# Optimization experiments

Measured on AMD Instinct MI355X. Metric: run time of the kernel, lower is better.

Reference implementation:

```python
import jax, jax.numpy as jnp
import numpy as np

B, S, D, H = 2, 2048, 1024, 16
DH = D // H
NEG = -1000000000.0


def setup_inputs() -> dict:
    key = jax.random.key(0)
    ks = jax.random.split(key, 8)
    q = jax.random.normal(ks[0], (B, S, D), dtype=jnp.float32)
    k = jax.random.normal(ks[1], (B, S, D), dtype=jnp.float32)
    v = jax.random.normal(ks[2], (B, S, D), dtype=jnp.float32)
    # padding mask [B, k_len]; ensure first key position is valid
    mask = jax.random.randint(ks[3], (B, S), 0, 2, dtype=jnp.int32)
    mask = mask.at[:, 0].set(1)
    scale = 1.0 / np.sqrt(D)
    Wq = jax.random.normal(ks[4], (D, D), dtype=jnp.float32) * scale
    Wk = jax.random.normal(ks[5], (D, D), dtype=jnp.float32) * scale
    Wv = jax.random.normal(ks[6], (D, D), dtype=jnp.float32) * scale
    Wo = jax.random.normal(ks[7], (D, D), dtype=jnp.float32) * scale
    return {"q": q, "k": k, "v": v, "mask": mask,
            "Wq": Wq, "Wk": Wk, "Wv": Wv, "Wo": Wo}


def reference(q, k, v, mask, Wq, Wk, Wv, Wo):
    # nn.Linear(bias=False): y = x @ W.T  (W is [out, in])
    Q = jnp.einsum('bsd,ed->bse', q, Wq)
    K = jnp.einsum('bsd,ed->bse', k, Wk)
    V = jnp.einsum('bsd,ed->bse', v, Wv)
    # split heads -> [B, H, S, DH]
    Q = Q.reshape(B, S, H, DH).transpose(0, 2, 1, 3)
    K = K.reshape(B, S, H, DH).transpose(0, 2, 1, 3)
    V = V.reshape(B, S, H, DH).transpose(0, 2, 1, 3)
    scores = jnp.einsum('bhqd,bhkd->bhqk', Q, K) / jnp.float32(np.sqrt(DH))
    # padding mask: [B, K] -> additive [B, 1, 1, K]
    pad = jnp.where(mask == 0, jnp.float32(NEG), jnp.float32(0.0))[:, None, None, :]
    scores = scores + pad
    # causal (mask_future=True): strict upper triangle blocked
    causal = jnp.where(jnp.triu(jnp.ones((S, S), dtype=bool), k=1),
                       jnp.float32(NEG), jnp.float32(0.0))
    scores = scores + causal
    attn = jax.nn.softmax(scores, axis=-1)
    out = jnp.einsum('bhqk,bhkd->bhqd', attn, V)  # [B, H, S, DH]
    out = out.transpose(0, 2, 1, 3).reshape(B, S, D)
    out = jnp.einsum('bsd,ed->bse', out, Wo)
    # dropout: identity in eval mode
    return out
```

## Files before the change

kernel.cpp:

```cpp
#include <hip/hip_runtime.h>
#include <stdint.h>

#define BB 2
#define SS 2048
#define DD 1024
#define HH 16
#define DHH 64

typedef __bf16 bf16_t;
typedef bf16_t bf16x8 __attribute__((ext_vector_type(8)));
typedef float f32x4 __attribute__((ext_vector_type(4)));
typedef short s16x4 __attribute__((ext_vector_type(4)));

union FragU { uint4 u; bf16x8 b; };
union Frag4U { uint2 u; s16x4 s; };

#if __has_builtin(__builtin_amdgcn_exp2f)
#define EXP2(x) __builtin_amdgcn_exp2f(x)
#else
#define EXP2(x) exp2f(x)
#endif

__device__ __forceinline__ unsigned short f2bf(float f) {
  union { float f; unsigned int u; } x; x.f = f;
  unsigned int u = x.u;
  return (unsigned short)((u + 0x7FFFu + ((u >> 16) & 1u)) >> 16);
}

__device__ __forceinline__ uint2 pack4(float4 v) {
  uint2 r;
  r.x = (unsigned)f2bf(v.x) | ((unsigned)f2bf(v.y) << 16);
  r.y = (unsigned)f2bf(v.z) | ((unsigned)f2bf(v.w) << 16);
  return r;
}

__device__ __forceinline__ bf16x8 ldsFrag(const unsigned short* s, int idx) {
  FragU f;
  f.u = *reinterpret_cast<const uint4*>(s + idx);
  return f.b;
}

__device__ __forceinline__ void gload_lds16(const unsigned short* g, unsigned short* s) {
  __builtin_amdgcn_global_load_lds(
      (const __attribute__((address_space(1))) unsigned int*)g,
      (__attribute__((address_space(3))) unsigned int*)s, 16, 0, 0);
}

#define MFMA16(a, b, c) __builtin_amdgcn_mfma_f32_16x16x32_bf16((a), (b), (c), 0, 0, 0)
#define MFMA16K16(a, b, c) __builtin_amdgcn_mfma_f32_16x16x16bf16_1k((a), (b), (c), 0, 0, 0)

__global__ __launch_bounds__(256) void convert_kernel(
    const float* __restrict__ q, const float* __restrict__ k, const float* __restrict__ v,
    const float* __restrict__ Wq, const float* __restrict__ Wk,
    const float* __restrict__ Wv, const float* __restrict__ Wo,
    const int* __restrict__ mask,
    unsigned short* __restrict__ Ab, unsigned short* __restrict__ Wb,
    float* __restrict__ Mf) {
  const int z = blockIdx.y;
  if (z == 7) {
    if (blockIdx.x >= 4) return;
    const size_t base = (size_t)blockIdx.x * 1024 + (size_t)threadIdx.x * 4;
    int4 m4 = *reinterpret_cast<const int4*>(mask + base);
    float4 p;
    p.x = (m4.x == 0) ? -1.0e9f : 0.0f;
    p.y = (m4.y == 0) ? -1.0e9f : 0.0f;
    p.z = (m4.z == 0) ? -1.0e9f : 0.0f;
    p.w = (m4.w == 0) ? -1.0e9f : 0.0f;
    *reinterpret_cast<float4*>(Mf + base) = p;
    return;
  }
  const float* src;
  unsigned short* dst;
  float scale = 1.0f;
  if (z < 3) {
    src = (z == 0) ? q : (z == 1) ? k : v;
    dst = Ab + (size_t)z * BB * SS * DD;
  } else {
    if (blockIdx.x >= (DD * DD / 1024)) return;
    src = (z == 3) ? Wq : (z == 4) ? Wk : (z == 5) ? Wv : Wo;
    dst = Wb + (size_t)(z - 3) * DD * DD;
    if (z == 3) scale = 0.125f * 1.44269504088896f;
  }
  const size_t base = (size_t)blockIdx.x * 1024 + (size_t)threadIdx.x * 4;
  float4 val = *reinterpret_cast<const float4*>(src + base);
  val.x *= scale; val.y *= scale; val.z *= scale; val.w *= scale;
  uint2 p = pack4(val);
  *reinterpret_cast<uint2*>(dst + base) = p;
}

__global__ __launch_bounds__(256) void proj128_kernel(
    const unsigned short* __restrict__ Ab, const unsigned short* __restrict__ Wb,
    unsigned short* __restrict__ Qb, unsigned short* __restrict__ Kb,
    unsigned short* __restrict__ Vt) {
  __shared__ unsigned short sA[128 * 64];
  __shared__ unsigned short sB[128 * 64];

  const int z = blockIdx.z;
  const unsigned short* A = Ab + (size_t)z * BB * SS * DD;
  const unsigned short* W = Wb + (size_t)z * DD * DD;
  unsigned short* Out = (z == 0) ? Qb : (z == 1) ? Kb : Vt;
  const int layout = (z == 2) ? 1 : 0;

  const int t = threadIdx.x;
  const int lane = t & 63, wave = t >> 6;
  const int quad = lane >> 4, l15 = lane & 15;
  const int wr = wave >> 1, wc = wave & 1;
  const int mBase = blockIdx.x * 128, nBase = blockIdx.y * 128;

  f32x4 acc[4][4] = {};

  for (int k0 = 0; k0 < DD; k0 += 64) {
    #pragma unroll
    for (int i = 0; i < 4; ++i) {
      const int g = wave * 4 + i;
      const int row = g * 8 + (lane >> 3);
      const int oct = (lane & 7) ^ (row & 7);
      gload_lds16(A + (size_t)(mBase + row) * DD + k0 + oct * 8, &sA[g * 512]);
      gload_lds16(W + (size_t)(nBase + row) * DD + k0 + oct * 8, &sB[g * 512]);
    }
    __syncthreads();

    #pragma unroll
    for (int kk = 0; kk < 2; ++kk) {
      bf16x8 af[4], bfr[4];
      #pragma unroll
      for (int i = 0; i < 4; ++i) {
        const int row = wr * 64 + i * 16 + l15;
        af[i] = ldsFrag(sA, (row * 8 + ((kk * 4 + quad) ^ (l15 & 7))) * 8);
      }
      #pragma unroll
      for (int j = 0; j < 4; ++j) {
        const int row = wc * 64 + j * 16 + l15;
        bfr[j] = ldsFrag(sB, (row * 8 + ((kk * 4 + quad) ^ (l15 & 7))) * 8);
      }
      #pragma unroll
      for (int i = 0; i < 4; ++i)
        #pragma unroll
        for (int j = 0; j < 4; ++j)
          acc[i][j] = MFMA16(af[i], bfr[j], acc[i][j]);
    }
    __syncthreads();
  }

  #pragma unroll
  for (int i = 0; i < 4; ++i) {
    #pragma unroll
    for (int j = 0; j < 4; ++j) {
      #pragma unroll
      for (int r = 0; r < 4; ++r) {
        int m = mBase + wr * 64 + i * 16 + quad * 4 + r;
        int n = nBase + wc * 64 + j * 16 + l15;
        int b = m >> 11, s = m & (SS - 1);
        int h = n >> 6, dh = n & (DHH - 1);
        size_t off;
        if (layout == 0)
          off = ((size_t)(b * HH + h) * SS + s) * DHH + dh;
        else
          off = ((size_t)(b * HH + h) * DHH + dh) * SS + s;
        Out[off] = f2bf(acc[i][j][r]);
      }
    }
  }
}

__global__ __launch_bounds__(256, 4) void attn_kernel(
    const unsigned short* __restrict__ Qb, const unsigned short* __restrict__ Kb,
    const unsigned short* __restrict__ Vt, const float* __restrict__ Mf,
    unsigned short* __restrict__ Ob) {
  __shared__ __align__(16) char smem[32768];
  unsigned short* sK = (unsigned short*)smem;
  unsigned short* sV = (unsigned short*)(smem + 16384);
  unsigned short* sO = (unsigned short*)smem;

  const int t = threadIdx.x;
  const int lane = t & 63, wave = t >> 6;
  const int quad = lane >> 4, l15 = lane & 15;

  const int id = blockIdx.x;
  const int xcd = id & 7, rest = id >> 3;
  const int hd = xcd * 4 + (rest >> 5);
  const int qt = 31 - (rest & 31);
  const int b = hd >> 4, h = hd & 15;
  const int qb = qt * 64;

  const size_t headOff = (size_t)hd * SS * DHH;
  const unsigned short* Qh = Qb + headOff;
  const unsigned short* Kh = Kb + headOff;
  const unsigned short* Vh = Vt + headOff;
  const float* Mp = Mf + b * SS;

  bf16x8 aq[2];
  {
    const unsigned short* qp = Qh + (size_t)(qb + wave * 16 + l15) * DHH + quad * 8;
    FragU f0, f1;
    f0.u = *reinterpret_cast<const uint4*>(qp);
    f1.u = *reinterpret_cast<const uint4*>(qp + 32);
    aq[0] = f0.b; aq[1] = f1.b;
  }

  float m_l = -1.0e30f, l_l = 0.0f;
  f32x4 oacc[4] = {};
  const int nc = (qt + 2) >> 1;
  const int qrow_abs = qb + wave * 16 + l15;

  for (int c = 0; c < nc; ++c) {
    const int c0 = c * 128;
    #pragma unroll
    for (int i = 0; i < 4; ++i) {
      const int g = wave * 4 + i;
      const int row = g * 8 + (lane >> 3);
      const int oct = (lane & 7) ^ (row & 7);
      gload_lds16(Kh + (size_t)(c0 + row) * DHH + oct * 8, &sK[g * 512]);
    }
    #pragma unroll
    for (int i = 0; i < 4; ++i) {
      const int g = wave * 4 + i;
      const int row = g * 4 + (lane >> 4);
      const int oct = (lane & 15) ^ (row & 15);
      gload_lds16(Vh + (size_t)row * SS + c0 + oct * 8, &sV[g * 512]);
    }
    __syncthreads();

    f32x4 sacc[8] = {};
    #pragma unroll
    for (int kk = 0; kk < 2; ++kk) {
      #pragma unroll
      for (int j = 0; j < 8; ++j) {
        const int row = j * 16 + l15;
        bf16x8 ak = ldsFrag(sK, (row * 8 + ((kk * 4 + quad) ^ (l15 & 7))) * 8);
        sacc[j] = MFMA16(ak, aq[kk], sacc[j]);
      }
    }

    float rm = -1.0e30f;
    #pragma unroll
    for (int j = 0; j < 8; ++j)
      rm = fmaxf(rm, fmaxf(fmaxf(sacc[j][0], sacc[j][1]), fmaxf(sacc[j][2], sacc[j][3])));
    rm = fmaxf(rm, __shfl_xor(rm, 16));
    rm = fmaxf(rm, __shfl_xor(rm, 32));
    const float mnew = fmaxf(m_l, rm);
    const float alpha = EXP2(m_l - mnew);
    m_l = mnew;

    const bool diag = (c == nc - 1);
    float rs = 0.0f;
    s16x4 pk[8];
    #pragma unroll
    for (int j = 0; j < 8; ++j) {
      float4 pf = *reinterpret_cast<const float4*>(Mp + c0 + j * 16 + quad * 4);
      float p0 = EXP2(sacc[j][0] - mnew + pf.x);
      float p1 = EXP2(sacc[j][1] - mnew + pf.y);
      float p2 = EXP2(sacc[j][2] - mnew + pf.z);
      float p3 = EXP2(sacc[j][3] - mnew + pf.w);
      if (diag) {
        const int key = c0 + j * 16 + quad * 4;
        p0 = (key + 0 > qrow_abs) ? 0.0f : p0;
        p1 = (key + 1 > qrow_abs) ? 0.0f : p1;
        p2 = (key + 2 > qrow_abs) ? 0.0f : p2;
        p3 = (key + 3 > qrow_abs) ? 0.0f : p3;
      }
      rs += (p0 + p1) + (p2 + p3);
      Frag4U fu;
      fu.u.x = __builtin_amdgcn_perm(__float_as_uint(p1) + 0x8000u,
                                     __float_as_uint(p0) + 0x8000u, 0x07060302u);
      fu.u.y = __builtin_amdgcn_perm(__float_as_uint(p3) + 0x8000u,
                                     __float_as_uint(p2) + 0x8000u, 0x07060302u);
      pk[j] = fu.s;
    }
    rs += __shfl_xor(rs, 16);
    rs += __shfl_xor(rs, 32);
    l_l = l_l * alpha + rs;

    #pragma unroll
    for (int jn = 0; jn < 4; ++jn)
      oacc[jn] *= alpha;

    #pragma unroll
    for (int j = 0; j < 8; ++j) {
      #pragma unroll
      for (int jn = 0; jn < 4; ++jn) {
        const int row = jn * 16 + l15;
        const int unit = row * 16 + ((2 * j + (quad >> 1)) ^ l15);
        Frag4U av;
        av.u = *reinterpret_cast<const uint2*>(&sV[unit * 8 + (quad & 1) * 4]);
        oacc[jn] = MFMA16K16(av.s, pk[j], oacc[jn]);
      }
    }
    __syncthreads();
  }

  const float inv = 1.0f / l_l;
  #pragma unroll
  for (int jn = 0; jn < 4; ++jn) {
    uint2 w;
    w.x = (unsigned)f2bf(oacc[jn][0] * inv) | ((unsigned)f2bf(oacc[jn][1] * inv) << 16);
    w.y = (unsigned)f2bf(oacc[jn][2] * inv) | ((unsigned)f2bf(oacc[jn][3] * inv) << 16);
    *reinterpret_cast<uint2*>(&sO[(wave * 16 + l15) * 72 + jn * 16 + quad * 4]) = w;
  }
  __syncthreads();
  {
    const int row = t >> 2, seg = t & 3;
    uint4 u0 = *reinterpret_cast<const uint4*>(&sO[row * 72 + seg * 16]);
    uint4 u1 = *reinterpret_cast<const uint4*>(&sO[row * 72 + seg * 16 + 8]);
    unsigned short* dst = Ob + (size_t)(b * SS + qb + row) * DD + h * DHH + seg * 16;
    *reinterpret_cast<uint4*>(dst) = u0;
    *reinterpret_cast<uint4*>(dst + 8) = u1;
  }
}

__global__ __launch_bounds__(256) void outproj_kernel(
    const unsigned short* __restrict__ Ag, const unsigned short* __restrict__ Wb,
    float* __restrict__ Out) {
  __shared__ unsigned short sA[128 * 64];
  __shared__ unsigned short sB[128 * 64];

  const unsigned short* W = Wb + (size_t)3 * DD * DD;
  const int t = threadIdx.x;
  const int lane = t & 63, wave = t >> 6;
  const int quad = lane >> 4, l15 = lane & 15;
  const int wr = wave >> 1, wc = wave & 1;
  const int mBase = blockIdx.x * 128, nBase = blockIdx.y * 128;

  f32x4 acc[4][4] = {};

  for (int k0 = 0; k0 < DD; k0 += 64) {
    #pragma unroll
    for (int i = 0; i < 4; ++i) {
      const int g = wave * 4 + i;
      const int row = g * 8 + (lane >> 3);
      const int oct = (lane & 7) ^ (row & 7);
      gload_lds16(Ag + (size_t)(mBase + row) * DD + k0 + oct * 8, &sA[g * 512]);
      gload_lds16(W + (size_t)(nBase + row) * DD + k0 + oct * 8, &sB[g * 512]);
    }
    __syncthreads();

    #pragma unroll
    for (int kk = 0; kk < 2; ++kk) {
      bf16x8 af[4], bfr[4];
      #pragma unroll
      for (int i = 0; i < 4; ++i) {
        const int row = wr * 64 + i * 16 + l15;
        af[i] = ldsFrag(sA, (row * 8 + ((kk * 4 + quad) ^ (l15 & 7))) * 8);
      }
      #pragma unroll
      for (int j = 0; j < 4; ++j) {
        const int row = wc * 64 + j * 16 + l15;
        bfr[j] = ldsFrag(sB, (row * 8 + ((kk * 4 + quad) ^ (l15 & 7))) * 8);
      }
      #pragma unroll
      for (int i = 0; i < 4; ++i)
        #pragma unroll
        for (int j = 0; j < 4; ++j)
          acc[i][j] = MFMA16(af[i], bfr[j], acc[i][j]);
    }
    __syncthreads();
  }

  #pragma unroll
  for (int i = 0; i < 4; ++i) {
    #pragma unroll
    for (int j = 0; j < 4; ++j) {
      #pragma unroll
      for (int r = 0; r < 4; ++r) {
        int m = mBase + wr * 64 + i * 16 + quad * 4 + r;
        int n = nBase + wc * 64 + j * 16 + l15;
        Out[(size_t)m * DD + n] = acc[i][j][r];
      }
    }
  }
}

extern "C" void kernel_launch(void* const* d_in, const int* in_sizes, int n_in,
                              void* d_out, int out_size, void* d_ws, size_t ws_size,
                              hipStream_t stream) {
  (void)in_sizes; (void)n_in; (void)out_size; (void)ws_size;
  const float* q  = (const float*)d_in[0];
  const float* k  = (const float*)d_in[1];
  const float* v  = (const float*)d_in[2];
  const int* mask = (const int*)d_in[3];
  const float* Wq = (const float*)d_in[4];
  const float* Wk = (const float*)d_in[5];
  const float* Wv = (const float*)d_in[6];
  const float* Wo = (const float*)d_in[7];
  float* out = (float*)d_out;

  const size_t AE = (size_t)BB * SS * DD;
  unsigned short* Ab = (unsigned short*)d_ws;
  unsigned short* Ob = Ab;
  unsigned short* Wb = Ab + 3 * AE;
  unsigned short* Qb = Wb + (size_t)4 * DD * DD;
  unsigned short* Kb = Qb + AE;
  unsigned short* Vt = Kb + AE;
  float* Mf = (float*)(Vt + AE);

  convert_kernel<<<dim3(AE / 1024, 8), 256, 0, stream>>>(
      q, k, v, Wq, Wk, Wv, Wo, mask, Ab, Wb, Mf);

  proj128_kernel<<<dim3(BB * SS / 128, DD / 128, 3), 256, 0, stream>>>(
      Ab, Wb, Qb, Kb, Vt);

  attn_kernel<<<dim3(32 * HH * BB), 256, 0, stream>>>(Qb, Kb, Vt, Mf, Ob);

  outproj_kernel<<<dim3(BB * SS / 128, DD / 128), 256, 0, stream>>>(Ob, Wb, out);
}
```

Baseline: 254.3 us.

## Double-buffer LDS in projection, attention and out-proj with smaller tiles

```diff
diff --git a/kernel.cpp b/kernel.cpp
--- a/kernel.cpp
+++ b/kernel.cpp
@@ -88,12 +88,12 @@
   *reinterpret_cast<uint2*>(dst + base) = p;
 }
 
-__global__ __launch_bounds__(256) void proj128_kernel(
+__global__ __launch_bounds__(256, 3) void proj_kernel(
     const unsigned short* __restrict__ Ab, const unsigned short* __restrict__ Wb,
     unsigned short* __restrict__ Qb, unsigned short* __restrict__ Kb,
     unsigned short* __restrict__ Vt) {
-  __shared__ unsigned short sA[128 * 64];
-  __shared__ unsigned short sB[128 * 64];
+  __shared__ unsigned short sA[2][64 * 64];
+  __shared__ unsigned short sB[2][128 * 64];
 
   const int z = blockIdx.z;
   const unsigned short* A = Ab + (size_t)z * BB * SS * DD;
@@ -105,50 +105,75 @@
   const int lane = t & 63, wave = t >> 6;
   const int quad = lane >> 4, l15 = lane & 15;
   const int wr = wave >> 1, wc = wave & 1;
-  const int mBase = blockIdx.x * 128, nBase = blockIdx.y * 128;
-
-  f32x4 acc[4][4] = {};
-
-  for (int k0 = 0; k0 < DD; k0 += 64) {
-    #pragma unroll
-    for (int i = 0; i < 4; ++i) {
-      const int g = wave * 4 + i;
-      const int row = g * 8 + (lane >> 3);
-      const int oct = (lane & 7) ^ (row & 7);
-      gload_lds16(A + (size_t)(mBase + row) * DD + k0 + oct * 8, &sA[g * 512]);
-      gload_lds16(W + (size_t)(nBase + row) * DD + k0 + oct * 8, &sB[g * 512]);
-    }
+  const int mBase = blockIdx.x * 64, nBase = blockIdx.y * 128;
+  const int srow = lane >> 3, soct = lane & 7;
+
+  f32x4 acc[2][4] = {};
+
+  #pragma unroll
+  for (int i = 0; i < 2; ++i) {
+    const int g = wave * 2 + i;
+    const int row = g * 8 + srow;
+    const int oct = soct ^ (row & 7);
+    gload_lds16(A + (size_t)(mBase + row) * DD + oct * 8, &sA[0][g * 512]);
+  }
+  #pragma unroll
+  for (int i = 0; i < 4; ++i) {
+    const int g = wave * 4 + i;
+    const int row = g * 8 + srow;
+    const int oct = soct ^ (row & 7);
+    gload_lds16(W + (size_t)(nBase + row) * DD + oct * 8, &sB[0][g * 512]);
+  }
+
+  for (int kt = 0; kt < DD / 64; ++kt) {
     __syncthreads();
-
+    if (kt + 1 < DD / 64) {
+      const int k1 = (kt + 1) * 64;
+      const int nb = (kt + 1) & 1;
+      #pragma unroll
+      for (int i = 0; i < 2; ++i) {
+        const int g = wave * 2 + i;
+        const int row = g * 8 + srow;
+        const int oct = soct ^ (row & 7);
+        gload_lds16(A + (size_t)(mBase + row) * DD + k1 + oct * 8, &sA[nb][g * 512]);
+      }
+      #pragma unroll
+      for (int i = 0; i < 4; ++i) {
+        const int g = wave * 4 + i;
+        const int row = g * 8 + srow;
+        const int oct = soct ^ (row & 7);
+        gload_lds16(W + (size_t)(nBase + row) * DD + k1 + oct * 8, &sB[nb][g * 512]);
+      }
+    }
+    const int cb = kt & 1;
     #pragma unroll
     for (int kk = 0; kk < 2; ++kk) {
-      bf16x8 af[4], bfr[4];
-      #pragma unroll
-      for (int i = 0; i < 4; ++i) {
-        const int row = wr * 64 + i * 16 + l15;
-        af[i] = ldsFrag(sA, (row * 8 + ((kk * 4 + quad) ^ (l15 & 7))) * 8);
+      bf16x8 af[2], bfr[4];
+      #pragma unroll
+      for (int i = 0; i < 2; ++i) {
+        const int row = wr * 32 + i * 16 + l15;
+        af[i] = ldsFrag(sA[cb], (row * 8 + ((kk * 4 + quad) ^ (l15 & 7))) * 8);
       }
       #pragma unroll
       for (int j = 0; j < 4; ++j) {
         const int row = wc * 64 + j * 16 + l15;
-        bfr[j] = ldsFrag(sB, (row * 8 + ((kk * 4 + quad) ^ (l15 & 7))) * 8);
-      }
-      #pragma unroll
-      for (int i = 0; i < 4; ++i)
+        bfr[j] = ldsFrag(sB[cb], (row * 8 + ((kk * 4 + quad) ^ (l15 & 7))) * 8);
+      }
+      #pragma unroll
+      for (int i = 0; i < 2; ++i)
         #pragma unroll
         for (int j = 0; j < 4; ++j)
           acc[i][j] = MFMA16(af[i], bfr[j], acc[i][j]);
     }
-    __syncthreads();
-  }
-
-  #pragma unroll
-  for (int i = 0; i < 4; ++i) {
+  }
+
+  #pragma unroll
+  for (int i = 0; i < 2; ++i) {
     #pragma unroll
     for (int j = 0; j < 4; ++j) {
       #pragma unroll
       for (int r = 0; r < 4; ++r) {
-        int m = mBase + wr * 64 + i * 16 + quad * 4 + r;
+        int m = mBase + wr * 32 + i * 16 + quad * 4 + r;
         int n = nBase + wc * 64 + j * 16 + l15;
         int b = m >> 11, s = m & (SS - 1);
         int h = n >> 6, dh = n & (DHH - 1);
@@ -166,11 +191,10 @@
 __global__ __launch_bounds__(256, 4) void attn_kernel(
     const unsigned short* __restrict__ Qb, const unsigned short* __restrict__ Kb,
     const unsigned short* __restrict__ Vt, const float* __restrict__ Mf,
-    unsigned short* __restrict__ Ob) {
-  __shared__ __align__(16) char smem[32768];
-  unsigned short* sK = (unsigned short*)smem;
-  unsigned short* sV = (unsigned short*)(smem + 16384);
-  unsigned short* sO = (unsigned short*)smem;
+    unsigned short* __restrict__ Obh) {
+  __shared__ __align__(16) unsigned short sK[2][64 * 64];
+  __shared__ __align__(16) unsigned short sV[2][64 * 64];
+  unsigned short* sO = &sK[0][0];
 
   const int t = threadIdx.x;
   const int lane = t & 63, wave = t >> 6;
@@ -180,7 +204,7 @@
   const int xcd = id & 7, rest = id >> 3;
   const int hd = xcd * 4 + (rest >> 5);
   const int qt = 31 - (rest & 31);
-  const int b = hd >> 4, h = hd & 15;
+  const int b = hd >> 4;
   const int qb = qt * 64;
 
   const size_t headOff = (size_t)hd * SS * DHH;
@@ -198,43 +222,52 @@
     aq[0] = f0.b; aq[1] = f1.b;
   }
 
+  const int srow = lane >> 3, soct = lane & 7;
+
+  #pragma unroll
+  for (int i = 0; i < 2; ++i) {
+    const int g = wave * 2 + i;
+    const int row = g * 8 + srow;
+    const int oct = soct ^ (row & 7);
+    gload_lds16(Kh + (size_t)row * DHH + oct * 8, &sK[0][g * 512]);
+    gload_lds16(Vh + (size_t)row * SS + oct * 8, &sV[0][g * 512]);
+  }
+
   float m_l = -1.0e30f, l_l = 0.0f;
   f32x4 oacc[4] = {};
-  const int nc = (qt + 2) >> 1;
   const int qrow_abs = qb + wave * 16 + l15;
 
-  for (int c = 0; c < nc; ++c) {
-    const int c0 = c * 128;
-    #pragma unroll
-    for (int i = 0; i < 4; ++i) {
-      const int g = wave * 4 + i;
-      const int row = g * 8 + (lane >> 3);
-      const int oct = (lane & 7) ^ (row & 7);
-      gload_lds16(Kh + (size_t)(c0 + row) * DHH + oct * 8, &sK[g * 512]);
-    }
-    #pragma unroll
-    for (int i = 0; i < 4; ++i) {
-      const int g = wave * 4 + i;
-      const int row = g * 4 + (lane >> 4);
-      const int oct = (lane & 15) ^ (row & 15);
-      gload_lds16(Vh + (size_t)row * SS + c0 + oct * 8, &sV[g * 512]);
-    }
+  for (int c = 0; c <= qt; ++c) {
     __syncthreads();
-
-    f32x4 sacc[8] = {};
+    if (c < qt) {
+      const int c1 = (c + 1) * 64;
+      const int nb = (c + 1) & 1;
+      #pragma unroll
+      for (int i = 0; i < 2; ++i) {
+        const int g = wave * 2 + i;
+        const int row = g * 8 + srow;
+        const int oct = soct ^ (row & 7);
+        gload_lds16(Kh + (size_t)(c1 + row) * DHH + oct * 8, &sK[nb][g * 512]);
+        gload_lds16(Vh + (size_t)row * SS + c1 + oct * 8, &sV[nb][g * 512]);
+      }
+    }
+    const int cb = c & 1;
+    const int c0 = c * 64;
+
+    f32x4 sacc[4] = {};
     #pragma unroll
     for (int kk = 0; kk < 2; ++kk) {
       #pragma unroll
-      for (int j = 0; j < 8; ++j) {
+      for (int j = 0; j < 4; ++j) {
         const int row = j * 16 + l15;
-        bf16x8 ak = ldsFrag(sK, (row * 8 + ((kk * 4 + quad) ^ (l15 & 7))) * 8);
+        bf16x8 ak = ldsFrag(sK[cb], (row * 8 + ((kk * 4 + quad) ^ (l15 & 7))) * 8);
         sacc[j] = MFMA16(ak, aq[kk], sacc[j]);
       }
     }
 
     float rm = -1.0e30f;
     #pragma unroll
-    for (int j = 0; j < 8; ++j)
+    for (int j = 0; j < 4; ++j)
       rm = fmaxf(rm, fmaxf(fmaxf(sacc[j][0], sacc[j][1]), fmaxf(sacc[j][2], sacc[j][3])));
     rm = fmaxf(rm, __shfl_xor(rm, 16));
     rm = fmaxf(rm, __shfl_xor(rm, 32));
@@ -242,11 +275,11 @@
     const float alpha = EXP2(m_l - mnew);
     m_l = mnew;
 
-    const bool diag = (c == nc - 1);
+    const bool diag = (c == qt);
     float rs = 0.0f;
-    s16x4 pk[8];
-    #pragma unroll
-    for (int j = 0; j < 8; ++j) {
+    s16x4 pk[4];
+    #pragma unroll
+    for (int j = 0; j < 4; ++j) {
       float4 pf = *reinterpret_cast<const float4*>(Mp + c0 + j * 16 + quad * 4);
       float p0 = EXP2(sacc[j][0] - mnew + pf.x);
       float p1 = EXP2(sacc[j][1] - mnew + pf.y);
@@ -276,19 +309,19 @@
       oacc[jn] *= alpha;
 
     #pragma unroll
-    for (int j = 0; j < 8; ++j) {
+    for (int j = 0; j < 4; ++j) {
       #pragma unroll
       for (int jn = 0; jn < 4; ++jn) {
         const int row = jn * 16 + l15;
-        const int unit = row * 16 + ((2 * j + (quad >> 1)) ^ l15);
+        const int oct = (2 * j + (quad >> 1)) ^ (l15 & 7);
         Frag4U av;
-        av.u = *reinterpret_cast<const uint2*>(&sV[unit * 8 + (quad & 1) * 4]);
+        av.u = *reinterpret_cast<const uint2*>(&sV[cb][(row * 8 + oct) * 8 + (quad & 1) * 4]);
         oacc[jn] = MFMA16K16(av.s, pk[j], oacc[jn]);
       }
     }
-    __syncthreads();
-  }
-
+  }
+
+  __syncthreads();
   const float inv = 1.0f / l_l;
   #pragma unroll
   for (int jn = 0; jn < 4; ++jn) {
@@ -302,67 +335,97 @@
     const int row = t >> 2, seg = t & 3;
     uint4 u0 = *reinterpret_cast<const uint4*>(&sO[row * 72 + seg * 16]);
     uint4 u1 = *reinterpret_cast<const uint4*>(&sO[row * 72 + seg * 16 + 8]);
-    unsigned short* dst = Ob + (size_t)(b * SS + qb + row) * DD + h * DHH + seg * 16;
+    unsigned short* dst = Obh + headOff + (size_t)(qb + row) * DHH + seg * 16;
     *reinterpret_cast<uint4*>(dst) = u0;
     *reinterpret_cast<uint4*>(dst + 8) = u1;
   }
 }
 
-__global__ __launch_bounds__(256) void outproj_kernel(
-    const unsigned short* __restrict__ Ag, const unsigned short* __restrict__ Wb,
+__global__ __launch_bounds__(256, 3) void outproj_kernel(
+    const unsigned short* __restrict__ Obh, const unsigned short* __restrict__ Wb,
     float* __restrict__ Out) {
-  __shared__ unsigned short sA[128 * 64];
-  __shared__ unsigned short sB[128 * 64];
+  __shared__ unsigned short sA[2][64 * 64];
+  __shared__ unsigned short sB[2][128 * 64];
 
   const unsigned short* W = Wb + (size_t)3 * DD * DD;
   const int t = threadIdx.x;
   const int lane = t & 63, wave = t >> 6;
   const int quad = lane >> 4, l15 = lane & 15;
   const int wr = wave >> 1, wc = wave & 1;
-  const int mBase = blockIdx.x * 128, nBase = blockIdx.y * 128;
-
-  f32x4 acc[4][4] = {};
-
-  for (int k0 = 0; k0 < DD; k0 += 64) {
-    #pragma unroll
-    for (int i = 0; i < 4; ++i) {
-      const int g = wave * 4 + i;
-      const int row = g * 8 + (lane >> 3);
-      const int oct = (lane & 7) ^ (row & 7);
-      gload_lds16(Ag + (size_t)(mBase + row) * DD + k0 + oct * 8, &sA[g * 512]);
-      gload_lds16(W + (size_t)(nBase + row) * DD + k0 + oct * 8, &sB[g * 512]);
-    }
+  const int mBase = blockIdx.x * 64, nBase = blockIdx.y * 128;
+  const int srow = lane >> 3, soct = lane & 7;
+
+  const int bidx = mBase >> 11;
+  const int sloc = mBase & (SS - 1);
+  const unsigned short* Abase = Obh + (size_t)bidx * HH * SS * DHH;
+
+  f32x4 acc[2][4] = {};
+
+  #pragma unroll
+  for (int i = 0; i < 2; ++i) {
+    const int g = wave * 2 + i;
+    const int row = g * 8 + srow;
+    const int oct = soct ^ (row & 7);
+    gload_lds16(Abase + ((size_t)0 * SS + sloc + row) * DHH + oct * 8, &sA[0][g * 512]);
+  }
+  #pragma unroll
+  for (int i = 0; i < 4; ++i) {
+    const int g = wave * 4 + i;
+    const int row = g * 8 + srow;
+    const int oct = soct ^ (row & 7);
+    gload_lds16(W + (size_t)(nBase + row) * DD + oct * 8, &sB[0][g * 512]);
+  }
+
+  for (int kt = 0; kt < HH; ++kt) {
     __syncthreads();
-
+    if (kt + 1 < HH) {
+      const int nb = (kt + 1) & 1;
+      #pragma unroll
+      for (int i = 0; i < 2; ++i) {
+        const int g = wave * 2 + i;
+        const int row = g * 8 + srow;
+        const int oct = soct ^ (row & 7);
+        gload_lds16(Abase + ((size_t)(kt + 1) * SS + sloc + row) * DHH + oct * 8,
+                    &sA[nb][g * 512]);
+      }
+      #pragma unroll
+      for (int i = 0; i < 4; ++i) {
+        const int g = wave * 4 + i;
+        const int row = g * 8 + srow;
+        const int oct = soct ^ (row & 7);
+        gload_lds16(W + (size_t)(nBase + row) * DD + (kt + 1) * 64 + oct * 8,
+                    &sB[nb][g * 512]);
+      }
+    }
+    const int cb = kt & 1;
     #pragma unroll
     for (int kk = 0; kk < 2; ++kk) {
-      bf16x8 af[4], bfr[4];
-      #pragma unroll
-      for (int i = 0; i < 4; ++i) {
-        const int row = wr * 64 + i * 16 + l15;
-        af[i] = ldsFrag(sA, (row * 8 + ((kk * 4 + quad) ^ (l15 & 7))) * 8);
+      bf16x8 af[2], bfr[4];
+      #pragma unroll
+      for (int i = 0; i < 2; ++i) {
+        const int row = wr * 32 + i * 16 + l15;
+        af[i] = ldsFrag(sA[cb], (row * 8 + ((kk * 4 + quad) ^ (l15 & 7))) * 8);
       }
       #pragma unroll
       for (int j = 0; j < 4; ++j) {
         const int row = wc * 64 + j * 16 + l15;
-        bfr[j] = ldsFrag(sB, (row * 8 + ((kk * 4 + quad) ^ (l15 & 7))) * 8);
-      }
-      #pragma unroll
-      for (int i = 0; i < 4; ++i)
+        bfr[j] = ldsFrag(sB[cb], (row * 8 + ((kk * 4 + quad) ^ (l15 & 7))) * 8);
+      }
+      #pragma unroll
+      for (int i = 0; i < 2; ++i)
         #pragma unroll
         for (int j = 0; j < 4; ++j)
           acc[i][j] = MFMA16(af[i], bfr[j], acc[i][j]);
     }
-    __syncthreads();
-  }
-
-  #pragma unroll
-  for (int i = 0; i < 4; ++i) {
+  }
+
+  #pragma unroll
+  for (int i = 0; i < 2; ++i) {
     #pragma unroll
     for (int j = 0; j < 4; ++j) {
       #pragma unroll
       for (int r = 0; r < 4; ++r) {
-        int m = mBase + wr * 64 + i * 16 + quad * 4 + r;
+        int m = mBase + wr * 32 + i * 16 + quad * 4 + r;
         int n = nBase + wc * 64 + j * 16 + l15;
         Out[(size_t)m * DD + n] = acc[i][j][r];
       }
@@ -385,21 +448,21 @@
   float* out = (float*)d_out;
 
   const size_t AE = (size_t)BB * SS * DD;
-  unsigned short* Ab = (unsigned short*)d_ws;
-  unsigned short* Ob = Ab;
-  unsigned short* Wb = Ab + 3 * AE;
-  unsigned short* Qb = Wb + (size_t)4 * DD * DD;
-  unsigned short* Kb = Qb + AE;
-  unsigned short* Vt = Kb + AE;
+  unsigned short* Ab  = (unsigned short*)d_ws;
+  unsigned short* Obh = Ab;
+  unsigned short* Wb  = Ab + 3 * AE;
+  unsigned short* Qb  = Wb + (size_t)4 * DD * DD;
+  unsigned short* Kb  = Qb + AE;
+  unsigned short* Vt  = Kb + AE;
   float* Mf = (float*)(Vt + AE);
 
   convert_kernel<<<dim3(AE / 1024, 8), 256, 0, stream>>>(
       q, k, v, Wq, Wk, Wv, Wo, mask, Ab, Wb, Mf);
 
-  proj128_kernel<<<dim3(BB * SS / 128, DD / 128, 3), 256, 0, stream>>>(
+  proj_kernel<<<dim3(BB * SS / 64, DD / 128, 3), 256, 0, stream>>>(
       Ab, Wb, Qb, Kb, Vt);
 
-  attn_kernel<<<dim3(32 * HH * BB), 256, 0, stream>>>(Qb, Kb, Vt, Mf, Ob);
-
-  outproj_kernel<<<dim3(BB * SS / 128, DD / 128), 256, 0, stream>>>(Ob, Wb, out);
-}
+  attn_kernel<<<dim3(32 * HH * BB), 256, 0, stream>>>(Qb, Kb, Vt, Mf, Obh);
+
+  outproj_kernel<<<dim3(BB * SS / 64, DD / 128), 256, 0, stream>>>(Obh, Wb, out);
+}
```

Result: faster. 241.9 us (-4.9%).

## Double-buffer K/V tiles in attention and write head-major output for out-projection

Applied to the files above, without the earlier changes.

```diff
diff --git a/kernel.cpp b/kernel.cpp
--- a/kernel.cpp
+++ b/kernel.cpp
@@ -166,11 +166,10 @@
 __global__ __launch_bounds__(256, 4) void attn_kernel(
     const unsigned short* __restrict__ Qb, const unsigned short* __restrict__ Kb,
     const unsigned short* __restrict__ Vt, const float* __restrict__ Mf,
-    unsigned short* __restrict__ Ob) {
-  __shared__ __align__(16) char smem[32768];
-  unsigned short* sK = (unsigned short*)smem;
-  unsigned short* sV = (unsigned short*)(smem + 16384);
-  unsigned short* sO = (unsigned short*)smem;
+    unsigned short* __restrict__ Obh) {
+  __shared__ __align__(16) unsigned short sK[2][64 * 64];
+  __shared__ __align__(16) unsigned short sV[2][64 * 64];
+  unsigned short* sO = &sK[0][0];
 
   const int t = threadIdx.x;
   const int lane = t & 63, wave = t >> 6;
@@ -178,9 +177,11 @@
 
   const int id = blockIdx.x;
   const int xcd = id & 7, rest = id >> 3;
-  const int hd = xcd * 4 + (rest >> 5);
-  const int qt = 31 - (rest & 31);
-  const int b = hd >> 4, h = hd & 15;
+  const int hg = rest >> 5;
+  const int hd = xcd * 4 + hg;
+  const int r5 = rest & 31;
+  const int qt = (hg & 1) ? (31 - r5) : r5;
+  const int b = hd >> 4;
   const int qb = qt * 64;
 
   const size_t headOff = (size_t)hd * SS * DHH;
@@ -198,43 +199,52 @@
     aq[0] = f0.b; aq[1] = f1.b;
   }
 
+  const int srow = lane >> 3, soct = lane & 7;
+
+  #pragma unroll
+  for (int i = 0; i < 2; ++i) {
+    const int g = wave * 2 + i;
+    const int row = g * 8 + srow;
+    const int oct = soct ^ (row & 7);
+    gload_lds16(Kh + (size_t)row * DHH + oct * 8, &sK[0][g * 512]);
+    gload_lds16(Vh + (size_t)row * SS + oct * 8, &sV[0][g * 512]);
+  }
+
   float m_l = -1.0e30f, l_l = 0.0f;
   f32x4 oacc[4] = {};
-  const int nc = (qt + 2) >> 1;
   const int qrow_abs = qb + wave * 16 + l15;
 
-  for (int c = 0; c < nc; ++c) {
-    const int c0 = c * 128;
-    #pragma unroll
-    for (int i = 0; i < 4; ++i) {
-      const int g = wave * 4 + i;
-      const int row = g * 8 + (lane >> 3);
-      const int oct = (lane & 7) ^ (row & 7);
-      gload_lds16(Kh + (size_t)(c0 + row) * DHH + oct * 8, &sK[g * 512]);
-    }
-    #pragma unroll
-    for (int i = 0; i < 4; ++i) {
-      const int g = wave * 4 + i;
-      const int row = g * 4 + (lane >> 4);
-      const int oct = (lane & 15) ^ (row & 15);
-      gload_lds16(Vh + (size_t)row * SS + c0 + oct * 8, &sV[g * 512]);
-    }
+  for (int c = 0; c <= qt; ++c) {
     __syncthreads();
-
-    f32x4 sacc[8] = {};
+    if (c < qt) {
+      const int c1 = (c + 1) * 64;
+      const int nb = (c + 1) & 1;
+      #pragma unroll
+      for (int i = 0; i < 2; ++i) {
+        const int g = wave * 2 + i;
+        const int row = g * 8 + srow;
+        const int oct = soct ^ (row & 7);
+        gload_lds16(Kh + (size_t)(c1 + row) * DHH + oct * 8, &sK[nb][g * 512]);
+        gload_lds16(Vh + (size_t)row * SS + c1 + oct * 8, &sV[nb][g * 512]);
+      }
+    }
+    const int cb = c & 1;
+    const int c0 = c * 64;
+
+    f32x4 sacc[4] = {};
     #pragma unroll
     for (int kk = 0; kk < 2; ++kk) {
       #pragma unroll
-      for (int j = 0; j < 8; ++j) {
+      for (int j = 0; j < 4; ++j) {
         const int row = j * 16 + l15;
-        bf16x8 ak = ldsFrag(sK, (row * 8 + ((kk * 4 + quad) ^ (l15 & 7))) * 8);
+        bf16x8 ak = ldsFrag(sK[cb], (row * 8 + ((kk * 4 + quad) ^ (l15 & 7))) * 8);
         sacc[j] = MFMA16(ak, aq[kk], sacc[j]);
       }
     }
 
     float rm = -1.0e30f;
     #pragma unroll
-    for (int j = 0; j < 8; ++j)
+    for (int j = 0; j < 4; ++j)
       rm = fmaxf(rm, fmaxf(fmaxf(sacc[j][0], sacc[j][1]), fmaxf(sacc[j][2], sacc[j][3])));
     rm = fmaxf(rm, __shfl_xor(rm, 16));
     rm = fmaxf(rm, __shfl_xor(rm, 32));
@@ -242,11 +252,11 @@
     const float alpha = EXP2(m_l - mnew);
     m_l = mnew;
 
-    const bool diag = (c == nc - 1);
+    const bool diag = (c == qt);
     float rs = 0.0f;
-    s16x4 pk[8];
-    #pragma unroll
-    for (int j = 0; j < 8; ++j) {
+    s16x4 pk[4];
+    #pragma unroll
+    for (int j = 0; j < 4; ++j) {
       float4 pf = *reinterpret_cast<const float4*>(Mp + c0 + j * 16 + quad * 4);
       float p0 = EXP2(sacc[j][0] - mnew + pf.x);
       float p1 = EXP2(sacc[j][1] - mnew + pf.y);
@@ -276,19 +286,19 @@
       oacc[jn] *= alpha;
 
     #pragma unroll
-    for (int j = 0; j < 8; ++j) {
+    for (int j = 0; j < 4; ++j) {
       #pragma unroll
       for (int jn = 0; jn < 4; ++jn) {
         const int row = jn * 16 + l15;
-        const int unit = row * 16 + ((2 * j + (quad >> 1)) ^ l15);
+        const int oct = (2 * j + (quad >> 1)) ^ (l15 & 7);
         Frag4U av;
-        av.u = *reinterpret_cast<const uint2*>(&sV[unit * 8 + (quad & 1) * 4]);
+        av.u = *reinterpret_cast<const uint2*>(&sV[cb][(row * 8 + oct) * 8 + (quad & 1) * 4]);
         oacc[jn] = MFMA16K16(av.s, pk[j], oacc[jn]);
       }
     }
-    __syncthreads();
-  }
-
+  }
+
+  __syncthreads();
   const float inv = 1.0f / l_l;
   #pragma unroll
   for (int jn = 0; jn < 4; ++jn) {
@@ -302,14 +312,14 @@
     const int row = t >> 2, seg = t & 3;
     uint4 u0 = *reinterpret_cast<const uint4*>(&sO[row * 72 + seg * 16]);
     uint4 u1 = *reinterpret_cast<const uint4*>(&sO[row * 72 + seg * 16 + 8]);
-    unsigned short* dst = Ob + (size_t)(b * SS + qb + row) * DD + h * DHH + seg * 16;
+    unsigned short* dst = Obh + headOff + (size_t)(qb + row) * DHH + seg * 16;
     *reinterpret_cast<uint4*>(dst) = u0;
     *reinterpret_cast<uint4*>(dst + 8) = u1;
   }
 }
 
 __global__ __launch_bounds__(256) void outproj_kernel(
-    const unsigned short* __restrict__ Ag, const unsigned short* __restrict__ Wb,
+    const unsigned short* __restrict__ Obh, const unsigned short* __restrict__ Wb,
     float* __restrict__ Out) {
   __shared__ unsigned short sA[128 * 64];
   __shared__ unsigned short sB[128 * 64];
@@ -321,16 +331,20 @@
   const int wr = wave >> 1, wc = wave & 1;
   const int mBase = blockIdx.x * 128, nBase = blockIdx.y * 128;
 
+  const int bidx = mBase >> 11;
+  const int sloc = mBase & (SS - 1);
+  const unsigned short* Abase = Obh + (size_t)bidx * HH * SS * DHH;
+
   f32x4 acc[4][4] = {};
 
-  for (int k0 = 0; k0 < DD; k0 += 64) {
+  for (int kt = 0; kt < HH; ++kt) {
     #pragma unroll
     for (int i = 0; i < 4; ++i) {
       const int g = wave * 4 + i;
       const int row = g * 8 + (lane >> 3);
       const int oct = (lane & 7) ^ (row & 7);
-      gload_lds16(Ag + (size_t)(mBase + row) * DD + k0 + oct * 8, &sA[g * 512]);
-      gload_lds16(W + (size_t)(nBase + row) * DD + k0 + oct * 8, &sB[g * 512]);
+      gload_lds16(Abase + ((size_t)kt * SS + sloc + row) * DHH + oct * 8, &sA[g * 512]);
+      gload_lds16(W + (size_t)(nBase + row) * DD + kt * 64 + oct * 8, &sB[g * 512]);
     }
     __syncthreads();
 
@@ -385,12 +399,12 @@
   float* out = (float*)d_out;
 
   const size_t AE = (size_t)BB * SS * DD;
-  unsigned short* Ab = (unsigned short*)d_ws;
-  unsigned short* Ob = Ab;
-  unsigned short* Wb = Ab + 3 * AE;
-  unsigned short* Qb = Wb + (size_t)4 * DD * DD;
-  unsigned short* Kb = Qb + AE;
-  unsigned short* Vt = Kb + AE;
+  unsigned short* Ab  = (unsigned short*)d_ws;
+  unsigned short* Obh = Ab;
+  unsigned short* Wb  = Ab + 3 * AE;
+  unsigned short* Qb  = Wb + (size_t)4 * DD * DD;
+  unsigned short* Kb  = Qb + AE;
+  unsigned short* Vt  = Kb + AE;
   float* Mf = (float*)(Vt + AE);
 
   convert_kernel<<<dim3(AE / 1024, 8), 256, 0, stream>>>(
@@ -399,7 +413,7 @@
   proj128_kernel<<<dim3(BB * SS / 128, DD / 128, 3), 256, 0, stream>>>(
       Ab, Wb, Qb, Kb, Vt);
 
-  attn_kernel<<<dim3(32 * HH * BB), 256, 0, stream>>>(Qb, Kb, Vt, Mf, Ob);
-
-  outproj_kernel<<<dim3(BB * SS / 128, DD / 128), 256, 0, stream>>>(Ob, Wb, out);
-}
+  attn_kernel<<<dim3(32 * HH * BB), 256, 0, stream>>>(Qb, Kb, Vt, Mf, Obh);
+
+  outproj_kernel<<<dim3(BB * SS / 128, DD / 128), 256, 0, stream>>>(Obh, Wb, out);
+}
```

Result: faster. 233.1 us (-8.4%).
